# Performance work log

Measured on AMD Instinct MI355X. Metric: run time of the kernel, lower is better.

Reference implementation:

```python
import jax, jax.numpy as jnp
import numpy as np

N_NODES = 131072      # total nodes across all graphs
IN_CHANNELS = 256     # node attribute dim after continuous WL embedding
NUM_PROJ = 256        # num_projections
NUM_QUANT = 256       # num_quantiles
NUM_GRAPHS = 256      # batch of graphs (equal-sized segments of 512 nodes)
P_NORM = 2            # p-sliced Wasserstein


def setup_inputs() -> dict:
    key = jax.random.key(0)
    k1, k2 = jax.random.split(key)
    x = jax.random.normal(k1, (N_NODES, IN_CHANNELS), dtype=jnp.float32)
    # fixed random projections, column-normalized (resample_projections)
    projections = jax.random.normal(k2, (IN_CHANNELS, NUM_PROJ), dtype=jnp.float32)
    projections = projections / jnp.sqrt(jnp.sum(projections ** 2, axis=0, keepdims=True))
    # cum_weights buffer: linspace(0, 1, num_quantiles)
    cum_weights = jnp.linspace(0.0, 1.0, NUM_QUANT, dtype=jnp.float32)
    # equal-sized graph segments (sorted segment ids), jit-friendly
    batch = (jnp.arange(N_NODES, dtype=jnp.int32) // (N_NODES // NUM_GRAPHS))
    return {
        "x": x,
        "projections": projections,
        "cum_weights": cum_weights,
        "batch": batch,
        "num_graphs": NUM_GRAPHS,
    }


def reference(x, projections, cum_weights, batch, num_graphs):
    # x: [N, C], projections: [C, P], cum_weights: [Q]
    n_nodes = x.shape[0]
    num_p = projections.shape[1]
    num_q = cum_weights.shape[0]
    nodes_per_graph = n_nodes // num_graphs

    xp = jnp.matmul(x, projections)                       # [N, P]
    xg = xp.reshape(num_graphs, nodes_per_graph, num_p)   # [B, n, P]
    xs = jnp.sort(xg, axis=1)                             # segmented sort per graph
    # torch.quantile(..., interpolation='lower'): index = floor(q * (n-1))
    idx = jnp.floor(cum_weights * (nodes_per_graph - 1)).astype(jnp.int32)  # [Q]
    quant = xs[:, idx, :]                                 # [B, Q, P]
    scale = (num_q * num_p) ** (1.0 / P_NORM)
    return quant.reshape(num_graphs, num_q * num_p) / scale
```

## Files before the change

kernel.cpp:

```cpp
#include <hip/hip_runtime.h>
#include <hip/hip_bf16.h>
#include <hip/hip_fp16.h>

typedef unsigned short u16;
typedef unsigned int u32;
typedef __bf16 bf16x8 __attribute__((ext_vector_type(8)));
typedef float f32x4 __attribute__((ext_vector_type(4)));
typedef u16 u16x8 __attribute__((ext_vector_type(8)));


__device__ __forceinline__ u16 f2bf(float f) {
  union { float f; u32 u; } v; v.f = f;
  u32 r = (v.u + 0x7FFFu + ((v.u >> 16) & 1u)) >> 16;
  return (u16)r;
}
__device__ __forceinline__ u32 pk_rne(float a, float b) {
  union { float f; u32 u; } va, vb; va.f = a; vb.f = b;
  u32 ra = (va.u + 0x7FFFu + ((va.u >> 16) & 1u)) >> 16;
  u32 rb = (vb.u + 0x7FFFu + ((vb.u >> 16) & 1u)) & 0xFFFF0000u;
  return rb | ra;
}

__device__ __forceinline__ void gl16(const void* g, void* l) {
  __builtin_amdgcn_global_load_lds((const __attribute__((address_space(1))) unsigned int*)g,
                                   (__attribute__((address_space(3))) unsigned int*)l,
                                   16, 0, 0);
}

__device__ __forceinline__ u32 pkmin(u32 a, u32 b) {
  u32 r; asm("v_pk_min_f16 %0, %1, %2" : "=v"(r) : "v"(a), "v"(b)); return r;
}
__device__ __forceinline__ u32 pkmax(u32 a, u32 b) {
  u32 r; asm("v_pk_max_f16 %0, %1, %2" : "=v"(r) : "v"(a), "v"(b)); return r;
}

template <int CTRL> __device__ __forceinline__ u32 xdpp(u32 x) {
  return (u32)__builtin_amdgcn_mov_dpp((int)x, CTRL, 0xF, 0xF, true);
}
template <int IMM> __device__ __forceinline__ u32 xswz(u32 x) {
  return (u32)__builtin_amdgcn_ds_swizzle((int)x, IMM);
}
#define EX_X1(x)  xdpp<0xB1>(x)
#define EX_X2(x)  xdpp<0x4E>(x)
#define EX_F3(x)  xdpp<0x1B>(x)
#define EX_F7(x)  xdpp<0x141>(x)
#define EX_F15(x) xdpp<0x140>(x)
#define EX_X8(x)  xdpp<0x128>(x)
#define EX_X4(x)  xswz<0x101F>(x)
#define EX_X16(x) xswz<0x401F>(x)
#define EX_F31(x) xswz<0x7C1F>(x)
#define EX_F63(x) ((u32)__shfl_xor((int)(x), 63, 64))

__global__ __launch_bounds__(256) void transpose_proj(const float* __restrict__ proj,
                                                      u16* __restrict__ projT) {
  const int k = blockIdx.x;
  const int p = threadIdx.x;
  projT[(size_t)p * 256 + k] = f2bf(proj[(size_t)k * 256 + p]);
}

__global__ __launch_bounds__(256) void gemm_xt(const float* __restrict__ x,
                                               const u16* __restrict__ projT,
                                               __half* __restrict__ xp16) {
  __shared__ u16 As[128 * 32];
  __shared__ float Bs[128 * 32];

  const int tid = threadIdx.x;
  const int bid = blockIdx.x;
  const int slot = bid & 7;
  const int j = bid >> 3;
  const int p0 = (j & 1) * 128;
  const int n0 = (slot + (j >> 1) * 8) * 128;
  const int lane = tid & 63;
  const int w = tid >> 6;
  const int wp = (w >> 1) * 64;
  const int wn = (w & 1) * 64;
  const int quad = lane >> 4;
  const int m16 = lane & 15;

  const u16* asrc0 = projT + (size_t)(p0 + (2 * w) * 16 + (lane >> 2)) * 256 + (lane & 3) * 8;
  const u16* asrc1 = asrc0 + 16 * 256;
  u16* adst0 = &As[(2 * w) * 512];
  u16* adst1 = &As[(2 * w + 1) * 512];
  const float* bsrc0 = x + (size_t)(n0 + (4 * w) * 8 + (lane >> 3)) * 256 + (lane & 7) * 4;
  const float* bsrc1 = bsrc0 + 8 * 256;
  const float* bsrc2 = bsrc0 + 16 * 256;
  const float* bsrc3 = bsrc0 + 24 * 256;
  float* bdst0 = &Bs[(4 * w) * 256];
  float* bdst1 = &Bs[(4 * w + 1) * 256];
  float* bdst2 = &Bs[(4 * w + 2) * 256];
  float* bdst3 = &Bs[(4 * w + 3) * 256];

  f32x4 acc[4][4];
#pragma unroll
  for (int i = 0; i < 4; ++i)
#pragma unroll
    for (int jj = 0; jj < 4; ++jj) acc[i][jj] = (f32x4){0.f, 0.f, 0.f, 0.f};

  for (int k0 = 0; k0 < 256; k0 += 32) {
    gl16(bsrc0 + k0, bdst0);
    gl16(bsrc1 + k0, bdst1);
    gl16(bsrc2 + k0, bdst2);
    gl16(bsrc3 + k0, bdst3);
    gl16(asrc0 + k0, adst0);
    gl16(asrc1 + k0, adst1);
    __syncthreads();

    bf16x8 af[4], bfv[4];
#pragma unroll
    for (int mi = 0; mi < 4; ++mi)
      af[mi] = *(const bf16x8*)&As[(wp + mi * 16 + m16) * 32 + quad * 8];
#pragma unroll
    for (int ni = 0; ni < 4; ++ni) {
      const float* bp = &Bs[(wn + ni * 16 + m16) * 32 + quad * 8];
      float4 f0 = *(const float4*)bp;
      float4 f1 = *(const float4*)(bp + 4);
      u32 pk[4] = { pk_rne(f0.x, f0.y), pk_rne(f0.z, f0.w),
                    pk_rne(f1.x, f1.y), pk_rne(f1.z, f1.w) };
      bfv[ni] = *(const bf16x8*)pk;
    }
#pragma unroll
    for (int mi = 0; mi < 4; ++mi)
#pragma unroll
      for (int ni = 0; ni < 4; ++ni)
        acc[mi][ni] = __builtin_amdgcn_mfma_f32_16x16x32_bf16(af[mi], bfv[ni], acc[mi][ni], 0, 0, 0);
    __syncthreads();
  }

#pragma unroll
  for (int mi = 0; mi < 4; ++mi) {
#pragma unroll
    for (int r = 0; r < 4; ++r) {
      const int p = p0 + wp + mi * 16 + quad * 4 + r;
      __half* dst = xp16 + (size_t)p * 131072 + (n0 + wn + m16);
#pragma unroll
      for (int ni = 0; ni < 4; ++ni) dst[ni * 16] = __float2half(acc[mi][ni][r]);
    }
  }
}

__global__ __launch_bounds__(1024) void sort_sel(const __half* __restrict__ xp16,
                                                 const float* __restrict__ cw,
                                                 float* __restrict__ out) {
  __shared__ u32 sbuf[16][520];
  const int tid = threadIdx.x;
  const int lane = tid & 63;
  const int w = tid >> 6;
  const int bid = blockIdx.x;
  const int g = bid >> 3;
  const int pt = bid & 7;
  const int p_lo = pt * 32 + w;
  const int p_hi = p_lo + 16;

  const u16* slo = (const u16*)(xp16 + (size_t)p_lo * 131072 + (size_t)g * 512) + lane * 8;
  const u16* shi = (const u16*)(xp16 + (size_t)p_hi * 131072 + (size_t)g * 512) + lane * 8;
  u16x8 lo = *(const u16x8*)slo;
  u16x8 hi = *(const u16x8*)shi;
  u32 v[8];
#pragma unroll
  for (int r = 0; r < 8; ++r) v[r] = (u32)lo[r] | ((u32)hi[r] << 16);

#define CE(i, j) { u32 mn_ = pkmin(v[i], v[j]); u32 mx_ = pkmax(v[i], v[j]); v[i] = mn_; v[j] = mx_; }
#define INTRA3 \
  CE(0,4) CE(1,5) CE(2,6) CE(3,7) \
  CE(0,2) CE(1,3) CE(4,6) CE(5,7) \
  CE(0,1) CE(2,3) CE(4,5) CE(6,7)

#define FLIPP(EX, lowbit) { \
    const bool low_ = (lane & (lowbit)) == 0; \
    u32 t_[8]; \
    _Pragma("unroll") for (int r = 0; r < 8; ++r) t_[r] = EX(v[7 - r]); \
    _Pragma("unroll") for (int r = 0; r < 8; ++r) { \
      u32 mn_ = pkmin(v[r], t_[r]); u32 mx_ = pkmax(v[r], t_[r]); \
      v[r] = low_ ? mn_ : mx_; } }

#define XCROSSP(EX, lm) { \
    const bool low_ = (lane & (lm)) == 0; \
    _Pragma("unroll") for (int r = 0; r < 8; ++r) { \
      u32 t_ = EX(v[r]); \
      u32 mn_ = pkmin(v[r], t_); u32 mx_ = pkmax(v[r], t_); \
      v[r] = low_ ? mn_ : mx_; } }

  CE(0,1) CE(2,3) CE(4,5) CE(6,7)
  CE(0,3) CE(1,2) CE(4,7) CE(5,6)
  CE(0,1) CE(2,3) CE(4,5) CE(6,7)
  CE(0,7) CE(1,6) CE(2,5) CE(3,4)
  CE(0,2) CE(1,3) CE(4,6) CE(5,7)
  CE(0,1) CE(2,3) CE(4,5) CE(6,7)
  FLIPP(EX_X1, 1)  INTRA3
  FLIPP(EX_F3, 2)  XCROSSP(EX_X1, 1)  INTRA3
  FLIPP(EX_F7, 4)  XCROSSP(EX_X2, 2) XCROSSP(EX_X1, 1)  INTRA3
  FLIPP(EX_F15, 8) XCROSSP(EX_X4, 4) XCROSSP(EX_X2, 2) XCROSSP(EX_X1, 1)  INTRA3
  FLIPP(EX_F31, 16) XCROSSP(EX_X8, 8) XCROSSP(EX_X4, 4) XCROSSP(EX_X2, 2) XCROSSP(EX_X1, 1)  INTRA3
  FLIPP(EX_F63, 32) XCROSSP(EX_X16, 16) XCROSSP(EX_X8, 8) XCROSSP(EX_X4, 4) XCROSSP(EX_X2, 2) XCROSSP(EX_X1, 1)  INTRA3

#undef CE
#undef INTRA3
#undef FLIPP
#undef XCROSSP

  *(uint4*)&sbuf[w][lane * 8]     = (uint4){v[0], v[1], v[2], v[3]};
  *(uint4*)&sbuf[w][lane * 8 + 4] = (uint4){v[4], v[5], v[6], v[7]};
  __syncthreads();

  const float scale = 1.0f / 256.0f;
#pragma unroll
  for (int it = 0; it < 8; ++it) {
    const int linear = it * 1024 + tid;
    const int q = linear >> 5;
    const int pl = linear & 31;
    const int iq = (int)floorf(cw[q] * 511.0f);
    const u32 val = sbuf[pl & 15][iq];
    const u16 h = (pl & 16) ? (u16)(val >> 16) : (u16)(val & 0xFFFF);
    __half_raw hr; hr.x = h;
    out[(size_t)g * 65536 + (size_t)q * 256 + pt * 32 + pl] = __half2float(__half(hr)) * scale;
  }
}

extern "C" void kernel_launch(void* const* d_in, const int* in_sizes, int n_in,
                              void* d_out, int out_size, void* d_ws, size_t ws_size,
                              hipStream_t stream) {
  const float* x    = (const float*)d_in[0];
  const float* proj = (const float*)d_in[1];
  const float* cw   = (const float*)d_in[2];
  float* out = (float*)d_out;

  __half* xp16 = (__half*)d_ws;
  u16* projT = (u16*)((char*)d_ws + (size_t)64 * 1024 * 1024);

  transpose_proj<<<256, 256, 0, stream>>>(proj, projT);
  gemm_xt<<<2048, 256, 0, stream>>>(x, projT, xp16);
  sort_sel<<<2048, 1024, 0, stream>>>(xp16, cw, out);
}
```

Measured before the change: 286.7 us.

## Fuse projection GEMM, segmented sort and quantile gather into one kernel

Replaces the three kernels (projection transpose, GEMM writing an fp16 intermediate to global memory, sort/select) with a single kernel per graph and half of the projections. The projection tile is converted to bf16 in LDS, the GEMM result is packed to fp16 pairs directly in LDS, and each wave sorts four column-pairs in place before gathering quantiles. This removes the 64MB global intermediate round trip and two launches. In exchange it uses about 130KB of LDS per block, leaving one block per CU with only 512 blocks. Each block also reconverts the projection matrix redundantly.

```diff
diff --git a/kernel.cpp b/kernel.cpp
--- a/kernel.cpp
+++ b/kernel.cpp
@@ -1,18 +1,17 @@
 #include <hip/hip_runtime.h>
-#include <hip/hip_bf16.h>
 #include <hip/hip_fp16.h>
 
 typedef unsigned short u16;
 typedef unsigned int u32;
 typedef __bf16 bf16x8 __attribute__((ext_vector_type(8)));
 typedef float f32x4 __attribute__((ext_vector_type(4)));
-typedef u16 u16x8 __attribute__((ext_vector_type(8)));
+typedef u32 u32x2 __attribute__((ext_vector_type(2)));
+typedef __fp16 half2v __attribute__((ext_vector_type(2)));
 
 
 __device__ __forceinline__ u16 f2bf(float f) {
   union { float f; u32 u; } v; v.f = f;
-  u32 r = (v.u + 0x7FFFu + ((v.u >> 16) & 1u)) >> 16;
-  return (u16)r;
+  return (u16)((v.u + 0x7FFFu + ((v.u >> 16) & 1u)) >> 16);
 }
 __device__ __forceinline__ u32 pk_rne(float a, float b) {
   union { float f; u32 u; } va, vb; va.f = a; vb.f = b;
@@ -20,20 +19,17 @@
   u32 rb = (vb.u + 0x7FFFu + ((vb.u >> 16) & 1u)) & 0xFFFF0000u;
   return rb | ra;
 }
-
 __device__ __forceinline__ void gl16(const void* g, void* l) {
   __builtin_amdgcn_global_load_lds((const __attribute__((address_space(1))) unsigned int*)g,
                                    (__attribute__((address_space(3))) unsigned int*)l,
                                    16, 0, 0);
 }
-
 __device__ __forceinline__ u32 pkmin(u32 a, u32 b) {
   u32 r; asm("v_pk_min_f16 %0, %1, %2" : "=v"(r) : "v"(a), "v"(b)); return r;
 }
 __device__ __forceinline__ u32 pkmax(u32 a, u32 b) {
   u32 r; asm("v_pk_max_f16 %0, %1, %2" : "=v"(r) : "v"(a), "v"(b)); return r;
 }
-
 template <int CTRL> __device__ __forceinline__ u32 xdpp(u32 x) {
   return (u32)__builtin_amdgcn_mov_dpp((int)x, CTRL, 0xF, 0xF, true);
 }
@@ -51,120 +47,92 @@
 #define EX_F31(x) xswz<0x7C1F>(x)
 #define EX_F63(x) ((u32)__shfl_xor((int)(x), 63, 64))
 
-__global__ __launch_bounds__(256) void transpose_proj(const float* __restrict__ proj,
-                                                      u16* __restrict__ projT) {
-  const int k = blockIdx.x;
-  const int p = threadIdx.x;
-  projT[(size_t)p * 256 + k] = f2bf(proj[(size_t)k * 256 + p]);
-}
-
-__global__ __launch_bounds__(256) void gemm_xt(const float* __restrict__ x,
-                                               const u16* __restrict__ projT,
-                                               __half* __restrict__ xp16) {
-  __shared__ u16 As[128 * 32];
-  __shared__ float Bs[128 * 32];
-
+#define LDS_BYTES 133120
+
+__global__ __launch_bounds__(1024, 4) void fused_swe(const float* __restrict__ x,
+                                                     const float* __restrict__ proj,
+                                                     const float* __restrict__ cw,
+                                                     float* __restrict__ out) {
+  __shared__ __align__(16) char smem[LDS_BYTES];
   const int tid = threadIdx.x;
-  const int bid = blockIdx.x;
-  const int slot = bid & 7;
-  const int j = bid >> 3;
-  const int p0 = (j & 1) * 128;
-  const int n0 = (slot + (j >> 1) * 8) * 128;
   const int lane = tid & 63;
   const int w = tid >> 6;
-  const int wp = (w >> 1) * 64;
-  const int wn = (w & 1) * 64;
-  const int quad = lane >> 4;
+  const int q4 = lane >> 4;
   const int m16 = lane & 15;
-
-  const u16* asrc0 = projT + (size_t)(p0 + (2 * w) * 16 + (lane >> 2)) * 256 + (lane & 3) * 8;
-  const u16* asrc1 = asrc0 + 16 * 256;
-  u16* adst0 = &As[(2 * w) * 512];
-  u16* adst1 = &As[(2 * w + 1) * 512];
-  const float* bsrc0 = x + (size_t)(n0 + (4 * w) * 8 + (lane >> 3)) * 256 + (lane & 7) * 4;
-  const float* bsrc1 = bsrc0 + 8 * 256;
-  const float* bsrc2 = bsrc0 + 16 * 256;
-  const float* bsrc3 = bsrc0 + 24 * 256;
-  float* bdst0 = &Bs[(4 * w) * 256];
-  float* bdst1 = &Bs[(4 * w + 1) * 256];
-  float* bdst2 = &Bs[(4 * w + 2) * 256];
-  float* bdst3 = &Bs[(4 * w + 3) * 256];
-
-  f32x4 acc[4][4];
-#pragma unroll
-  for (int i = 0; i < 4; ++i)
-#pragma unroll
-    for (int jj = 0; jj < 4; ++jj) acc[i][jj] = (f32x4){0.f, 0.f, 0.f, 0.f};
-
-  for (int k0 = 0; k0 < 256; k0 += 32) {
-    gl16(bsrc0 + k0, bdst0);
-    gl16(bsrc1 + k0, bdst1);
-    gl16(bsrc2 + k0, bdst2);
-    gl16(bsrc3 + k0, bdst3);
-    gl16(asrc0 + k0, adst0);
-    gl16(asrc1 + k0, adst1);
+  const int bid = blockIdx.x;
+  const int g = bid & 255;
+  const int ph = bid >> 8;
+
+  float* Xb = (float*)smem;
+  u16* Ab = (u16*)(smem + 65536);
+  u32* sb = (u32*)smem;
+
+#pragma unroll
+  for (int i = 0; i < 8; ++i) {
+    const int id = tid + i * 1024;
+    const int k = id >> 5;
+    const int pg = (id & 31) * 4;
+    float4 f = *(const float4*)(proj + (size_t)k * 256 + ph * 128 + pg);
+    Ab[(pg + 0) * 264 + k] = f2bf(f.x);
+    Ab[(pg + 1) * 264 + k] = f2bf(f.y);
+    Ab[(pg + 2) * 264 + k] = f2bf(f.z);
+    Ab[(pg + 3) * 264 + k] = f2bf(f.w);
+  }
+
+  const float* xsrc = x + ((size_t)g * 512 + (tid >> 3)) * 256 + (tid & 7) * 4;
+  char* xdst = (char*)smem + w * 1024;
+
+  f32x4 acc[2][8];
+#pragma unroll
+  for (int nt = 0; nt < 2; ++nt)
+#pragma unroll
+    for (int pt = 0; pt < 8; ++pt) acc[nt][pt] = (f32x4){0.f, 0.f, 0.f, 0.f};
+
+  for (int ch = 0; ch < 8; ++ch) {
+    const int k0 = ch * 32;
+#pragma unroll
+    for (int c = 0; c < 4; ++c)
+      gl16(xsrc + (size_t)c * 128 * 256 + k0, xdst + c * 16384);
     __syncthreads();
 
-    bf16x8 af[4], bfv[4];
-#pragma unroll
-    for (int mi = 0; mi < 4; ++mi)
-      af[mi] = *(const bf16x8*)&As[(wp + mi * 16 + m16) * 32 + quad * 8];
-#pragma unroll
-    for (int ni = 0; ni < 4; ++ni) {
-      const float* bp = &Bs[(wn + ni * 16 + m16) * 32 + quad * 8];
+    bf16x8 bfr[2];
+#pragma unroll
+    for (int nt = 0; nt < 2; ++nt) {
+      const float* bp = Xb + (w * 32 + nt * 16 + m16) * 32 + q4 * 8;
       float4 f0 = *(const float4*)bp;
       float4 f1 = *(const float4*)(bp + 4);
       u32 pk[4] = { pk_rne(f0.x, f0.y), pk_rne(f0.z, f0.w),
                     pk_rne(f1.x, f1.y), pk_rne(f1.z, f1.w) };
-      bfv[ni] = *(const bf16x8*)pk;
+      bfr[nt] = *(const bf16x8*)pk;
     }
 #pragma unroll
-    for (int mi = 0; mi < 4; ++mi)
-#pragma unroll
-      for (int ni = 0; ni < 4; ++ni)
-        acc[mi][ni] = __builtin_amdgcn_mfma_f32_16x16x32_bf16(af[mi], bfv[ni], acc[mi][ni], 0, 0, 0);
+    for (int pt = 0; pt < 8; ++pt) {
+      bf16x8 af = *(const bf16x8*)&Ab[(pt * 16 + m16) * 264 + k0 + q4 * 8];
+      acc[0][pt] = __builtin_amdgcn_mfma_f32_16x16x32_bf16(af, bfr[0], acc[0][pt], 0, 0, 0);
+      acc[1][pt] = __builtin_amdgcn_mfma_f32_16x16x32_bf16(af, bfr[1], acc[1][pt], 0, 0, 0);
+    }
     __syncthreads();
   }
 
 #pragma unroll
-  for (int mi = 0; mi < 4; ++mi) {
-#pragma unroll
-    for (int r = 0; r < 4; ++r) {
-      const int p = p0 + wp + mi * 16 + quad * 4 + r;
-      __half* dst = xp16 + (size_t)p * 131072 + (n0 + wn + m16);
-#pragma unroll
-      for (int ni = 0; ni < 4; ++ni) dst[ni * 16] = __float2half(acc[mi][ni][r]);
-    }
-  }
-}
-
-__global__ __launch_bounds__(1024) void sort_sel(const __half* __restrict__ xp16,
-                                                 const float* __restrict__ cw,
-                                                 float* __restrict__ out) {
-  __shared__ u32 sbuf[16][520];
-  const int tid = threadIdx.x;
-  const int lane = tid & 63;
-  const int w = tid >> 6;
-  const int bid = blockIdx.x;
-  const int g = bid >> 3;
-  const int pt = bid & 7;
-  const int p_lo = pt * 32 + w;
-  const int p_hi = p_lo + 16;
-
-  const u16* slo = (const u16*)(xp16 + (size_t)p_lo * 131072 + (size_t)g * 512) + lane * 8;
-  const u16* shi = (const u16*)(xp16 + (size_t)p_hi * 131072 + (size_t)g * 512) + lane * 8;
-  u16x8 lo = *(const u16x8*)slo;
-  u16x8 hi = *(const u16x8*)shi;
-  u32 v[8];
-#pragma unroll
-  for (int r = 0; r < 8; ++r) v[r] = (u32)lo[r] | ((u32)hi[r] << 16);
+  for (int nt = 0; nt < 2; ++nt)
+#pragma unroll
+    for (int pt4 = 0; pt4 < 4; ++pt4)
+#pragma unroll
+      for (int r = 0; r < 4; ++r) {
+        union { half2v h; u32 u; } cv;
+        cv.h = __builtin_amdgcn_cvt_pkrtz(acc[nt][pt4][r], acc[nt][pt4 + 4][r]);
+        const int pcol = pt4 * 16 + q4 * 4 + r;
+        const int n = w * 32 + nt * 16 + m16;
+        sb[pcol * 518 + n] = cv.u;
+      }
+  __syncthreads();
 
 #define CE(i, j) { u32 mn_ = pkmin(v[i], v[j]); u32 mx_ = pkmax(v[i], v[j]); v[i] = mn_; v[j] = mx_; }
 #define INTRA3 \
   CE(0,4) CE(1,5) CE(2,6) CE(3,7) \
   CE(0,2) CE(1,3) CE(4,6) CE(5,7) \
   CE(0,1) CE(2,3) CE(4,5) CE(6,7)
-
 #define FLIPP(EX, lowbit) { \
     const bool low_ = (lane & (lowbit)) == 0; \
     u32 t_[8]; \
@@ -172,7 +140,6 @@
     _Pragma("unroll") for (int r = 0; r < 8; ++r) { \
       u32 mn_ = pkmin(v[r], t_[r]); u32 mx_ = pkmax(v[r], t_[r]); \
       v[r] = low_ ? mn_ : mx_; } }
-
 #define XCROSSP(EX, lm) { \
     const bool low_ = (lane & (lm)) == 0; \
     _Pragma("unroll") for (int r = 0; r < 8; ++r) { \
@@ -180,39 +147,47 @@
       u32 mn_ = pkmin(v[r], t_); u32 mx_ = pkmax(v[r], t_); \
       v[r] = low_ ? mn_ : mx_; } }
 
-  CE(0,1) CE(2,3) CE(4,5) CE(6,7)
-  CE(0,3) CE(1,2) CE(4,7) CE(5,6)
-  CE(0,1) CE(2,3) CE(4,5) CE(6,7)
-  CE(0,7) CE(1,6) CE(2,5) CE(3,4)
-  CE(0,2) CE(1,3) CE(4,6) CE(5,7)
-  CE(0,1) CE(2,3) CE(4,5) CE(6,7)
-  FLIPP(EX_X1, 1)  INTRA3
-  FLIPP(EX_F3, 2)  XCROSSP(EX_X1, 1)  INTRA3
-  FLIPP(EX_F7, 4)  XCROSSP(EX_X2, 2) XCROSSP(EX_X1, 1)  INTRA3
-  FLIPP(EX_F15, 8) XCROSSP(EX_X4, 4) XCROSSP(EX_X2, 2) XCROSSP(EX_X1, 1)  INTRA3
-  FLIPP(EX_F31, 16) XCROSSP(EX_X8, 8) XCROSSP(EX_X4, 4) XCROSSP(EX_X2, 2) XCROSSP(EX_X1, 1)  INTRA3
-  FLIPP(EX_F63, 32) XCROSSP(EX_X16, 16) XCROSSP(EX_X8, 8) XCROSSP(EX_X4, 4) XCROSSP(EX_X2, 2) XCROSSP(EX_X1, 1)  INTRA3
-
+  for (int s = 0; s < 4; ++s) {
+    u32* col = sb + (w * 4 + s) * 518;
+    u32 v[8];
+#pragma unroll
+    for (int r2 = 0; r2 < 4; ++r2)
+      *(u32x2*)&v[r2 * 2] = *(const u32x2*)&col[lane * 8 + r2 * 2];
+
+    CE(0,1) CE(2,3) CE(4,5) CE(6,7)
+    CE(0,3) CE(1,2) CE(4,7) CE(5,6)
+    CE(0,1) CE(2,3) CE(4,5) CE(6,7)
+    CE(0,7) CE(1,6) CE(2,5) CE(3,4)
+    CE(0,2) CE(1,3) CE(4,6) CE(5,7)
+    CE(0,1) CE(2,3) CE(4,5) CE(6,7)
+    FLIPP(EX_X1, 1)  INTRA3
+    FLIPP(EX_F3, 2)  XCROSSP(EX_X1, 1)  INTRA3
+    FLIPP(EX_F7, 4)  XCROSSP(EX_X2, 2) XCROSSP(EX_X1, 1)  INTRA3
+    FLIPP(EX_F15, 8) XCROSSP(EX_X4, 4) XCROSSP(EX_X2, 2) XCROSSP(EX_X1, 1)  INTRA3
+    FLIPP(EX_F31, 16) XCROSSP(EX_X8, 8) XCROSSP(EX_X4, 4) XCROSSP(EX_X2, 2) XCROSSP(EX_X1, 1)  INTRA3
+    FLIPP(EX_F63, 32) XCROSSP(EX_X16, 16) XCROSSP(EX_X8, 8) XCROSSP(EX_X4, 4) XCROSSP(EX_X2, 2) XCROSSP(EX_X1, 1)  INTRA3
+
+#pragma unroll
+    for (int r2 = 0; r2 < 4; ++r2)
+      *(u32x2*)&col[lane * 8 + r2 * 2] = *(const u32x2*)&v[r2 * 2];
+  }
 #undef CE
 #undef INTRA3
 #undef FLIPP
 #undef XCROSSP
-
-  *(uint4*)&sbuf[w][lane * 8]     = (uint4){v[0], v[1], v[2], v[3]};
-  *(uint4*)&sbuf[w][lane * 8 + 4] = (uint4){v[4], v[5], v[6], v[7]};
   __syncthreads();
 
   const float scale = 1.0f / 256.0f;
-#pragma unroll
-  for (int it = 0; it < 8; ++it) {
+#pragma unroll 4
+  for (int it = 0; it < 32; ++it) {
     const int linear = it * 1024 + tid;
-    const int q = linear >> 5;
-    const int pl = linear & 31;
+    const int q = linear >> 7;
+    const int pl = linear & 127;
     const int iq = (int)floorf(cw[q] * 511.0f);
-    const u32 val = sbuf[pl & 15][iq];
-    const u16 h = (pl & 16) ? (u16)(val >> 16) : (u16)(val & 0xFFFF);
+    const u32 val = sb[(pl & 63) * 518 + iq];
+    const u16 h = (pl & 64) ? (u16)(val >> 16) : (u16)(val & 0xFFFF);
     __half_raw hr; hr.x = h;
-    out[(size_t)g * 65536 + (size_t)q * 256 + pt * 32 + pl] = __half2float(__half(hr)) * scale;
+    out[(size_t)g * 65536 + (size_t)q * 256 + ph * 128 + pl] = __half2float(__half(hr)) * scale;
   }
 }
 
@@ -223,11 +198,7 @@
   const float* proj = (const float*)d_in[1];
   const float* cw   = (const float*)d_in[2];
   float* out = (float*)d_out;
-
-  __half* xp16 = (__half*)d_ws;
-  u16* projT = (u16*)((char*)d_ws + (size_t)64 * 1024 * 1024);
-
-  transpose_proj<<<256, 256, 0, stream>>>(proj, projT);
-  gemm_xt<<<2048, 256, 0, stream>>>(x, projT, xp16);
-  sort_sel<<<2048, 1024, 0, stream>>>(xp16, cw, out);
-}
+  (void)d_ws; (void)ws_size;
+
+  fused_swe<<<512, 1024, 0, stream>>>(x, proj, cw, out);
+}
```

Measured after the change: 298.3 us. 1.04x slower.
